# Performance work log

Measured on AMD Instinct MI355X. Metric: run time of the kernel, lower is better.

Reference implementation:

```python
import jax, jax.numpy as jnp
import numpy as np

HIDDEN = 4096
INTER = 11008
GROUP = 128
B, S = 1, 2048


def setup_inputs() -> dict:
    key = jax.random.key(0)
    ks = jax.random.split(key, 10)
    inp = {
        "x": jax.random.normal(ks[0], (B, S, HIDDEN), dtype=jnp.float32),
        "gate_qw": jax.random.randint(ks[1], (INTER, HIDDEN), 0, 16, dtype=jnp.int32),
        "gate_qz": jax.random.randint(ks[2], (INTER, HIDDEN // GROUP), 0, 16, dtype=jnp.int32),
        "gate_scale": jax.random.uniform(ks[3], (INTER, HIDDEN // GROUP), dtype=jnp.float32) * 0.02,
        "gate_bias": jnp.zeros((INTER,), dtype=jnp.float32),
        "up_qw": jax.random.randint(ks[4], (INTER, HIDDEN), 0, 16, dtype=jnp.int32),
        "up_qz": jax.random.randint(ks[5], (INTER, HIDDEN // GROUP), 0, 16, dtype=jnp.int32),
        "up_scale": jax.random.uniform(ks[6], (INTER, HIDDEN // GROUP), dtype=jnp.float32) * 0.02,
        "up_bias": jnp.zeros((INTER,), dtype=jnp.float32),
        "down_qw": jax.random.randint(ks[7], (HIDDEN, INTER), 0, 16, dtype=jnp.int32),
        "down_qz": jax.random.randint(ks[8], (HIDDEN, INTER // GROUP), 0, 16, dtype=jnp.int32),
        "down_scale": jax.random.uniform(ks[9], (HIDDEN, INTER // GROUP), dtype=jnp.float32) * 0.02,
        "down_bias": jnp.zeros((HIDDEN,), dtype=jnp.float32),
        "group_size": GROUP,
    }
    return inp


def _dequant(qw, qz, scale, group_size):
    # qw: [O, I] int codes in [0,16); qz, scale: [O, I//g]
    O, I = qw.shape
    g = group_size
    q = qw.reshape(O, I // g, g).astype(jnp.float32)
    w = (q - qz[:, :, None].astype(jnp.float32)) * scale[:, :, None]
    return w.reshape(O, I)  # [O, I]


def reference(x, gate_qw, gate_qz, gate_scale, gate_bias,
              up_qw, up_qz, up_scale, up_bias,
              down_qw, down_qz, down_scale, down_bias, group_size):
    Wg = _dequant(gate_qw, gate_qz, gate_scale, group_size)   # [INTER, HIDDEN]
    Wu = _dequant(up_qw, up_qz, up_scale, group_size)         # [INTER, HIDDEN]
    Wd = _dequant(down_qw, down_qz, down_scale, group_size)   # [HIDDEN, INTER]
    g = jnp.einsum('bsh,ih->bsi', x, Wg) + gate_bias          # [B,S,INTER]
    u = jnp.einsum('bsh,ih->bsi', x, Wu) + up_bias            # [B,S,INTER]
    h = jax.nn.silu(g) * u                                    # SwiGLU
    y = jnp.einsum('bsi,hi->bsh', h, Wd) + down_bias          # [B,S,HIDDEN]
    return y
```

## Files before the change

### kernel.cpp

```cpp
#include <hip/hip_runtime.h>
#include <hip/hip_bf16.h>
#include <stdint.h>

#define SEQ    2048
#define HIDDEN 4096
#define INTER  11008

typedef short bf16x8 __attribute__((ext_vector_type(8)));
typedef float f32x4  __attribute__((ext_vector_type(4)));
typedef unsigned short u16x8 __attribute__((ext_vector_type(8)));

__device__ __forceinline__ unsigned short f2bf(float f) {
    union { __hip_bfloat16 h; unsigned short u; } v;
    v.h = __float2bfloat16(f);
    return v.u;
}

__device__ __forceinline__ void gload_lds16(const void* g, void* lds) {
    __builtin_amdgcn_global_load_lds(
        (const __attribute__((address_space(1))) uint32_t*)g,
        (__attribute__((address_space(3))) uint32_t*)lds,
        16, 0, 0);
}

__global__ __launch_bounds__(256) void k_cvt_x(const float* __restrict__ x,
                                               unsigned short* __restrict__ xb) {
    int i = (blockIdx.x * 256 + threadIdx.x) * 4;
    float4 v = *(const float4*)(x + i);
    ushort4 o;
    o.x = f2bf(v.x); o.y = f2bf(v.y); o.z = f2bf(v.z); o.w = f2bf(v.w);
    *(ushort4*)(xb + i) = o;
}

__global__ __launch_bounds__(256) void k_dequant(
    const int* __restrict__ qw, const int* __restrict__ qz,
    const float* __restrict__ sc, unsigned short* __restrict__ w)
{
    size_t i = ((size_t)blockIdx.x * 256 + threadIdx.x) * 8;
    int gi = (int)(i >> 7);
    int   z = qz[gi];
    float s = sc[gi];
    float zs = -(float)z * s;
    int4 q0 = *(const int4*)(qw + i);
    int4 q1 = *(const int4*)(qw + i + 4);
    u16x8 o;
    o[0] = f2bf(fmaf((float)q0.x, s, zs));
    o[1] = f2bf(fmaf((float)q0.y, s, zs));
    o[2] = f2bf(fmaf((float)q0.z, s, zs));
    o[3] = f2bf(fmaf((float)q0.w, s, zs));
    o[4] = f2bf(fmaf((float)q1.x, s, zs));
    o[5] = f2bf(fmaf((float)q1.y, s, zs));
    o[6] = f2bf(fmaf((float)q1.z, s, zs));
    o[7] = f2bf(fmaf((float)q1.w, s, zs));
    *(u16x8*)(w + i) = o;
}

__global__ __launch_bounds__(512) void k_gate_up(
    const unsigned short* __restrict__ xb,
    const unsigned short* __restrict__ wg,
    const unsigned short* __restrict__ wu,
    const float* __restrict__ gbias, const float* __restrict__ ubias,
    unsigned short* __restrict__ h)
{
    __shared__ __align__(16) unsigned short At[256 * 64];
    __shared__ __align__(16) unsigned short Bg[128 * 64];
    __shared__ __align__(16) unsigned short Bu[128 * 64];

    const int bid = blockIdx.x;
    const int mt  = bid & 7;
    const int nt  = bid >> 3;
    const int m0  = mt * 256;
    const int n0  = nt * 128;

    const int t    = threadIdx.x;
    const int lane = t & 63;
    const int wave = t >> 6;
    const int wm = (wave >> 1) * 64;
    const int wn = (wave & 1) * 64;

    f32x4 accG[4][4], accU[4][4];
#pragma unroll
    for (int mi = 0; mi < 4; ++mi)
#pragma unroll
        for (int ni = 0; ni < 4; ++ni) {
            accG[mi][ni] = (f32x4){0.f, 0.f, 0.f, 0.f};
            accU[mi][ni] = (f32x4){0.f, 0.f, 0.f, 0.f};
        }

    for (int kt = 0; kt < HIDDEN / 64; ++kt) {
        const int k0 = kt * 64;

#pragma unroll
        for (int cc = 0; cc < 4; ++cc) {
            int idx  = t + 512 * cc;
            int row  = idx >> 3;
            int scol = ((idx & 7) * 16) ^ ((row & 7) << 4);
            gload_lds16((const char*)(xb + (size_t)(m0 + row) * HIDDEN + k0) + scol,
                        (char*)At + idx * 16);
        }
#pragma unroll
        for (int cc = 0; cc < 2; ++cc) {
            int idx  = t + 512 * cc;
            int row  = idx >> 3;
            int scol = ((idx & 7) * 16) ^ ((row & 7) << 4);
            gload_lds16((const char*)(wg + (size_t)(n0 + row) * HIDDEN + k0) + scol,
                        (char*)Bg + idx * 16);
            gload_lds16((const char*)(wu + (size_t)(n0 + row) * HIDDEN + k0) + scol,
                        (char*)Bu + idx * 16);
        }

        __syncthreads();

#pragma unroll
        for (int kk = 0; kk < 2; ++kk) {
            bf16x8 af[4], bg[4], bu[4];
            int colb = kk * 64 + ((lane >> 4) * 16);
#pragma unroll
            for (int mi = 0; mi < 4; ++mi) {
                int row = wm + mi * 16 + (lane & 15);
                af[mi] = *(const bf16x8*)((const char*)At + row * 128 +
                                          (colb ^ ((row & 7) << 4)));
            }
#pragma unroll
            for (int ni = 0; ni < 4; ++ni) {
                int row = wn + ni * 16 + (lane & 15);
                int off = row * 128 + (colb ^ ((row & 7) << 4));
                bg[ni] = *(const bf16x8*)((const char*)Bg + off);
                bu[ni] = *(const bf16x8*)((const char*)Bu + off);
            }
            __builtin_amdgcn_s_setprio(1);
#pragma unroll
            for (int mi = 0; mi < 4; ++mi)
#pragma unroll
                for (int ni = 0; ni < 4; ++ni) {
                    accG[mi][ni] = __builtin_amdgcn_mfma_f32_16x16x32_bf16(
                        af[mi], bg[ni], accG[mi][ni], 0, 0, 0);
                    accU[mi][ni] = __builtin_amdgcn_mfma_f32_16x16x32_bf16(
                        af[mi], bu[ni], accU[mi][ni], 0, 0, 0);
                }
            __builtin_amdgcn_s_setprio(0);
        }

        __syncthreads();
    }

#pragma unroll
    for (int ni = 0; ni < 4; ++ni) {
        int col = n0 + wn + ni * 16 + (lane & 15);
        float gb = gbias[col], ub = ubias[col];
#pragma unroll
        for (int mi = 0; mi < 4; ++mi) {
#pragma unroll
            for (int j = 0; j < 4; ++j) {
                int row = m0 + wm + mi * 16 + ((lane >> 4) * 4) + j;
                float g = accG[mi][ni][j] + gb;
                float u = accU[mi][ni][j] + ub;
                float sig = 1.f / (1.f + __expf(-g));
                h[(size_t)row * INTER + col] = f2bf(g * sig * u);
            }
        }
    }
}

__global__ __launch_bounds__(512) void k_down(
    const unsigned short* __restrict__ h,
    const unsigned short* __restrict__ wd,
    const float* __restrict__ dbias,
    float* __restrict__ y)
{
    __shared__ __align__(16) unsigned short At[128 * 64];
    __shared__ __align__(16) unsigned short Bd[128 * 64];

    const int bid = blockIdx.x;
    const int mt  = bid & 15;
    const int nt  = bid >> 4;
    const int m0  = mt * 128;
    const int n0  = nt * 128;

    const int t    = threadIdx.x;
    const int lane = t & 63;
    const int wave = t >> 6;
    const int wm = (wave >> 2) * 64;
    const int wn = (wave & 3) * 32;

    f32x4 acc[4][2];
#pragma unroll
    for (int mi = 0; mi < 4; ++mi)
#pragma unroll
        for (int ni = 0; ni < 2; ++ni)
            acc[mi][ni] = (f32x4){0.f, 0.f, 0.f, 0.f};

    for (int kt = 0; kt < INTER / 64; ++kt) {
        const int k0 = kt * 64;

#pragma unroll
        for (int cc = 0; cc < 2; ++cc) {
            int idx  = t + 512 * cc;
            int row  = idx >> 3;
            int scol = ((idx & 7) * 16) ^ ((row & 7) << 4);
            gload_lds16((const char*)(h + (size_t)(m0 + row) * INTER + k0) + scol,
                        (char*)At + idx * 16);
            gload_lds16((const char*)(wd + (size_t)(n0 + row) * INTER + k0) + scol,
                        (char*)Bd + idx * 16);
        }

        __syncthreads();

#pragma unroll
        for (int kk = 0; kk < 2; ++kk) {
            bf16x8 af[4], bd[2];
#pragma unroll
            for (int mi = 0; mi < 4; ++mi) {
                int row  = wm + mi * 16 + (lane & 15);
                int colb = kk * 64 + ((lane >> 4) * 16);
                af[mi] = *(const bf16x8*)((const char*)At + row * 128 +
                                          (colb ^ ((row & 7) << 4)));
            }
#pragma unroll
            for (int ni = 0; ni < 2; ++ni) {
                int row  = wn + ni * 16 + (lane & 15);
                int colb = kk * 64 + ((lane >> 4) * 16);
                bd[ni] = *(const bf16x8*)((const char*)Bd + row * 128 +
                                          (colb ^ ((row & 7) << 4)));
            }
            __builtin_amdgcn_s_setprio(1);
#pragma unroll
            for (int mi = 0; mi < 4; ++mi)
#pragma unroll
                for (int ni = 0; ni < 2; ++ni)
                    acc[mi][ni] = __builtin_amdgcn_mfma_f32_16x16x32_bf16(
                        af[mi], bd[ni], acc[mi][ni], 0, 0, 0);
            __builtin_amdgcn_s_setprio(0);
        }

        __syncthreads();
    }

#pragma unroll
    for (int ni = 0; ni < 2; ++ni) {
        int col = n0 + wn + ni * 16 + (lane & 15);
        float db = dbias[col];
#pragma unroll
        for (int mi = 0; mi < 4; ++mi) {
#pragma unroll
            for (int j = 0; j < 4; ++j) {
                int row = m0 + wm + mi * 16 + ((lane >> 4) * 4) + j;
                y[(size_t)row * HIDDEN + col] = acc[mi][ni][j] + db;
            }
        }
    }
}

extern "C" void kernel_launch(void* const* d_in, const int* in_sizes, int n_in,
                              void* d_out, int out_size, void* d_ws, size_t ws_size,
                              hipStream_t stream) {
    const float* x    = (const float*)d_in[0];
    const int*   gqw  = (const int*)d_in[1];
    const int*   gqz  = (const int*)d_in[2];
    const float* gsc  = (const float*)d_in[3];
    const float* gbia = (const float*)d_in[4];
    const int*   uqw  = (const int*)d_in[5];
    const int*   uqz  = (const int*)d_in[6];
    const float* usc  = (const float*)d_in[7];
    const float* ubia = (const float*)d_in[8];
    const int*   dqw  = (const int*)d_in[9];
    const int*   dqz  = (const int*)d_in[10];
    const float* dsc  = (const float*)d_in[11];
    const float* dbia = (const float*)d_in[12];
    float* y = (float*)d_out;

    const size_t N_XB = (size_t)SEQ * HIDDEN;
    const size_t N_H  = (size_t)SEQ * INTER;
    const size_t N_W  = (size_t)INTER * HIDDEN;

    unsigned short* xb  = (unsigned short*)d_ws;
    unsigned short* hh  = xb + N_XB;
    unsigned short* wgb = hh + N_H;
    unsigned short* wub = wgb + N_W;
    unsigned short* wdb = wgb;

    const int dq_blocks = (int)(N_W / 2048);

    k_cvt_x<<<(SEQ * HIDDEN) / 1024, 256, 0, stream>>>(x, xb);
    k_dequant<<<dq_blocks, 256, 0, stream>>>(gqw, gqz, gsc, wgb);
    k_dequant<<<dq_blocks, 256, 0, stream>>>(uqw, uqz, usc, wub);
    k_gate_up<<<dim3(688), 512, 0, stream>>>(xb, wgb, wub, gbia, ubia, hh);
    k_dequant<<<dq_blocks, 256, 0, stream>>>(dqw, dqz, dsc, wdb);
    k_down<<<dim3(512), 512, 0, stream>>>(hh, wdb, dbia, y);
}
```

Before: 845.9 us.

## Fuse prep kernels, shrink gate-up tile, overlap down dequant with gate-up

Merges the x conversion and the gate/up dequant into one launch. The gate-up GEMM tile shrinks from 256x128 to 128x128 so there are more blocks. When the workspace is large enough, the down-weight dequant runs as extra blocks appended to the gate-up grid, so it overlaps the GEMM tail instead of running as a separate serial kernel. Block-index swizzles are added to both GEMMs for L2 locality. The smaller tile lowers A-tile reuse per block, and the appended dequant blocks may compete with GEMM blocks for CUs.

Measured after the change: 700.8 us (median of 3 runs). 1.21x faster.

```diff
diff --git a/kernel.cpp b/kernel.cpp
--- a/kernel.cpp
+++ b/kernel.cpp
@@ -23,20 +23,12 @@
         16, 0, 0);
 }
 
-__global__ __launch_bounds__(256) void k_cvt_x(const float* __restrict__ x,
-                                               unsigned short* __restrict__ xb) {
-    int i = (blockIdx.x * 256 + threadIdx.x) * 4;
-    float4 v = *(const float4*)(x + i);
-    ushort4 o;
-    o.x = f2bf(v.x); o.y = f2bf(v.y); o.z = f2bf(v.z); o.w = f2bf(v.w);
-    *(ushort4*)(xb + i) = o;
-}
-
-__global__ __launch_bounds__(256) void k_dequant(
+__device__ __forceinline__ void deq_block(
     const int* __restrict__ qw, const int* __restrict__ qz,
-    const float* __restrict__ sc, unsigned short* __restrict__ w)
-{
-    size_t i = ((size_t)blockIdx.x * 256 + threadIdx.x) * 8;
+    const float* __restrict__ sc, unsigned short* __restrict__ w,
+    int db, int t)
+{
+    size_t i = (size_t)db * 4096 + (size_t)t * 8;
     int gi = (int)(i >> 7);
     int   z = qz[gi];
     float s = sc[gi];
@@ -55,34 +47,73 @@
     *(u16x8*)(w + i) = o;
 }
 
+__global__ __launch_bounds__(512) void k_prep(
+    const float* __restrict__ x, unsigned short* __restrict__ xb,
+    const int* __restrict__ gqw, const int* __restrict__ gqz,
+    const float* __restrict__ gsc, unsigned short* __restrict__ wgb,
+    const int* __restrict__ uqw, const int* __restrict__ uqz,
+    const float* __restrict__ usc, unsigned short* __restrict__ wub)
+{
+    const int bid = blockIdx.x;
+    const int t   = threadIdx.x;
+    if (bid < 2048) {
+        size_t i = ((size_t)bid * 512 + t) * 8;
+        float4 v0 = *(const float4*)(x + i);
+        float4 v1 = *(const float4*)(x + i + 4);
+        u16x8 o;
+        o[0] = f2bf(v0.x); o[1] = f2bf(v0.y); o[2] = f2bf(v0.z); o[3] = f2bf(v0.w);
+        o[4] = f2bf(v1.x); o[5] = f2bf(v1.y); o[6] = f2bf(v1.z); o[7] = f2bf(v1.w);
+        *(u16x8*)(xb + i) = o;
+    } else if (bid < 13056) {
+        deq_block(gqw, gqz, gsc, wgb, bid - 2048, t);
+    } else {
+        deq_block(uqw, uqz, usc, wub, bid - 13056, t);
+    }
+}
+
+__global__ __launch_bounds__(512) void k_deq_fb(
+    const int* __restrict__ qw, const int* __restrict__ qz,
+    const float* __restrict__ sc, unsigned short* __restrict__ w)
+{
+    deq_block(qw, qz, sc, w, blockIdx.x, threadIdx.x);
+}
+
 __global__ __launch_bounds__(512) void k_gate_up(
     const unsigned short* __restrict__ xb,
     const unsigned short* __restrict__ wg,
     const unsigned short* __restrict__ wu,
     const float* __restrict__ gbias, const float* __restrict__ ubias,
-    unsigned short* __restrict__ h)
-{
-    __shared__ __align__(16) unsigned short At[256 * 64];
+    unsigned short* __restrict__ h,
+    const int* __restrict__ dqw, const int* __restrict__ dqz,
+    const float* __restrict__ dsc, unsigned short* __restrict__ wdb)
+{
+    __shared__ __align__(16) unsigned short At[128 * 64];
     __shared__ __align__(16) unsigned short Bg[128 * 64];
     __shared__ __align__(16) unsigned short Bu[128 * 64];
 
-    const int bid = blockIdx.x;
-    const int mt  = bid & 7;
-    const int nt  = bid >> 3;
-    const int m0  = mt * 256;
-    const int n0  = nt * 128;
+    if (blockIdx.x >= 1376) {
+        deq_block(dqw, dqz, dsc, wdb, blockIdx.x - 1376, threadIdx.x);
+        return;
+    }
+
+    const int orig = blockIdx.x;
+    const int swz  = (orig & 7) * 172 + (orig >> 3);
+    const int mt   = swz & 15;
+    const int nt   = swz >> 4;
+    const int m0   = mt * 128;
+    const int n0   = nt * 128;
 
     const int t    = threadIdx.x;
     const int lane = t & 63;
     const int wave = t >> 6;
-    const int wm = (wave >> 1) * 64;
-    const int wn = (wave & 1) * 64;
-
-    f32x4 accG[4][4], accU[4][4];
+    const int wm = (wave >> 2) * 64;
+    const int wn = (wave & 3) * 32;
+
+    f32x4 accG[4][2], accU[4][2];
 #pragma unroll
     for (int mi = 0; mi < 4; ++mi)
 #pragma unroll
-        for (int ni = 0; ni < 4; ++ni) {
+        for (int ni = 0; ni < 2; ++ni) {
             accG[mi][ni] = (f32x4){0.f, 0.f, 0.f, 0.f};
             accU[mi][ni] = (f32x4){0.f, 0.f, 0.f, 0.f};
         }
@@ -91,18 +122,12 @@
         const int k0 = kt * 64;
 
 #pragma unroll
-        for (int cc = 0; cc < 4; ++cc) {
+        for (int cc = 0; cc < 2; ++cc) {
             int idx  = t + 512 * cc;
             int row  = idx >> 3;
             int scol = ((idx & 7) * 16) ^ ((row & 7) << 4);
             gload_lds16((const char*)(xb + (size_t)(m0 + row) * HIDDEN + k0) + scol,
                         (char*)At + idx * 16);
-        }
-#pragma unroll
-        for (int cc = 0; cc < 2; ++cc) {
-            int idx  = t + 512 * cc;
-            int row  = idx >> 3;
-            int scol = ((idx & 7) * 16) ^ ((row & 7) << 4);
             gload_lds16((const char*)(wg + (size_t)(n0 + row) * HIDDEN + k0) + scol,
                         (char*)Bg + idx * 16);
             gload_lds16((const char*)(wu + (size_t)(n0 + row) * HIDDEN + k0) + scol,
@@ -113,18 +138,19 @@
 
 #pragma unroll
         for (int kk = 0; kk < 2; ++kk) {
-            bf16x8 af[4], bg[4], bu[4];
-            int colb = kk * 64 + ((lane >> 4) * 16);
+            bf16x8 af[4], bg[2], bu[2];
 #pragma unroll
             for (int mi = 0; mi < 4; ++mi) {
-                int row = wm + mi * 16 + (lane & 15);
+                int row  = wm + mi * 16 + (lane & 15);
+                int colb = kk * 64 + ((lane >> 4) * 16);
                 af[mi] = *(const bf16x8*)((const char*)At + row * 128 +
                                           (colb ^ ((row & 7) << 4)));
             }
 #pragma unroll
-            for (int ni = 0; ni < 4; ++ni) {
-                int row = wn + ni * 16 + (lane & 15);
-                int off = row * 128 + (colb ^ ((row & 7) << 4));
+            for (int ni = 0; ni < 2; ++ni) {
+                int row  = wn + ni * 16 + (lane & 15);
+                int colb = kk * 64 + ((lane >> 4) * 16);
+                int off  = row * 128 + (colb ^ ((row & 7) << 4));
                 bg[ni] = *(const bf16x8*)((const char*)Bg + off);
                 bu[ni] = *(const bf16x8*)((const char*)Bu + off);
             }
@@ -132,7 +158,7 @@
 #pragma unroll
             for (int mi = 0; mi < 4; ++mi)
 #pragma unroll
-                for (int ni = 0; ni < 4; ++ni) {
+                for (int ni = 0; ni < 2; ++ni) {
                     accG[mi][ni] = __builtin_amdgcn_mfma_f32_16x16x32_bf16(
                         af[mi], bg[ni], accG[mi][ni], 0, 0, 0);
                     accU[mi][ni] = __builtin_amdgcn_mfma_f32_16x16x32_bf16(
@@ -145,7 +171,7 @@
     }
 
 #pragma unroll
-    for (int ni = 0; ni < 4; ++ni) {
+    for (int ni = 0; ni < 2; ++ni) {
         int col = n0 + wn + ni * 16 + (lane & 15);
         float gb = gbias[col], ub = ubias[col];
 #pragma unroll
@@ -171,11 +197,12 @@
     __shared__ __align__(16) unsigned short At[128 * 64];
     __shared__ __align__(16) unsigned short Bd[128 * 64];
 
-    const int bid = blockIdx.x;
-    const int mt  = bid & 15;
-    const int nt  = bid >> 4;
-    const int m0  = mt * 128;
-    const int n0  = nt * 128;
+    const int orig = blockIdx.x;
+    const int swz  = (orig & 7) * 64 + (orig >> 3);
+    const int mt   = swz & 15;
+    const int nt   = swz >> 4;
+    const int m0   = mt * 128;
+    const int n0   = nt * 128;
 
     const int t    = threadIdx.x;
     const int lane = t & 63;
@@ -277,14 +304,23 @@
     unsigned short* hh  = xb + N_XB;
     unsigned short* wgb = hh + N_H;
     unsigned short* wub = wgb + N_W;
-    unsigned short* wdb = wgb;
-
-    const int dq_blocks = (int)(N_W / 2048);
-
-    k_cvt_x<<<(SEQ * HIDDEN) / 1024, 256, 0, stream>>>(x, xb);
-    k_dequant<<<dq_blocks, 256, 0, stream>>>(gqw, gqz, gsc, wgb);
-    k_dequant<<<dq_blocks, 256, 0, stream>>>(uqw, uqz, usc, wub);
-    k_gate_up<<<dim3(688), 512, 0, stream>>>(xb, wgb, wub, gbia, ubia, hh);
-    k_dequant<<<dq_blocks, 256, 0, stream>>>(dqw, dqz, dsc, wdb);
-    k_down<<<dim3(512), 512, 0, stream>>>(hh, wdb, dbia, y);
-}
+
+    const size_t need_big = (N_XB + N_H + 3 * N_W) * sizeof(unsigned short);
+    const bool   big      = ws_size >= need_big;
+
+    k_prep<<<dim3(24064), 512, 0, stream>>>(x, xb, gqw, gqz, gsc, wgb,
+                                            uqw, uqz, usc, wub);
+
+    if (big) {
+        unsigned short* wdb = wub + N_W;
+        k_gate_up<<<dim3(1376 + 11008), 512, 0, stream>>>(
+            xb, wgb, wub, gbia, ubia, hh, dqw, dqz, dsc, wdb);
+        k_down<<<dim3(512), 512, 0, stream>>>(hh, wdb, dbia, y);
+    } else {
+        unsigned short* wdb = wgb;
+        k_gate_up<<<dim3(1376), 512, 0, stream>>>(
+            xb, wgb, wub, gbia, ubia, hh, dqw, dqz, dsc, wdb);
+        k_deq_fb<<<dim3(11008), 512, 0, stream>>>(dqw, dqz, dsc, wdb);
+        k_down<<<dim3(512), 512, 0, stream>>>(hh, wdb, dbia, y);
+    }
+}
```
